# Performance work log

Hardware: AMD Instinct MI355X
Metric: run time of the kernel (lower is better)

The kernel has to match this reference:

```python
import jax, jax.numpy as jnp
import numpy as np

# DeepSeek MLA prefill pipeline (absorbed form), matching the GEMM/bmm/sparse-attention
# Dims: m=512 tokens, hidden=7168, d_kv_c=512, d_q_c=1536, d_r=64, d_q=d_kv=128,
# h=16 local heads, attention dim d = d_kv_c + d_r = 576, s_kv=4096, topk=512.

M, HID = 512, 7168
D_KV_C, D_Q_C, D_R, D_Q, D_KV = 512, 1536, 64, 128, 128
H = 16
S_KV, TOPK = 4096, 512
D_ATT = D_KV_C + D_R  # 576


def setup_inputs() -> dict:
    key = jax.random.key(0)
    ks = jax.random.split(key, 8)
    s = lambda n: 1.0 / np.sqrt(n).astype(np.float32)
    return {
        "x": jax.random.normal(ks[0], (M, HID), jnp.float32),
        "W_cqkv": jax.random.normal(ks[1], (HID, D_KV_C + D_Q_C + D_R), jnp.float32) * s(HID),
        "W_uq": jax.random.normal(ks[2], (D_Q_C, H * (D_Q + D_R)), jnp.float32) * s(D_Q_C),
        "W_qk": jax.random.normal(ks[3], (H, D_Q, D_KV_C), jnp.float32) * s(D_Q),
        "kv_cache": jax.random.normal(ks[4], (S_KV, D_ATT), jnp.float32),
        "W_o1": jax.random.normal(ks[5], (H, D_KV_C, D_KV), jnp.float32) * s(D_KV_C),
        "W_oproj": jax.random.normal(ks[6], (H * D_KV, HID), jnp.float32) * s(H * D_KV),
        "indices": jax.random.randint(ks[7], (M, TOPK), 0, S_KV, jnp.int32),
    }


def reference(x, W_cqkv, W_uq, W_qk, kv_cache, W_o1, W_oproj, indices):
    # 1) QKV compression GEMM: [m, hid] @ [hid, d_kv_c + d_q_c + d_r]
    c = x @ W_cqkv
    kv_c_new = c[:, :D_KV_C]                      # compressed KV (would extend cache)
    q_c = c[:, D_KV_C:D_KV_C + D_Q_C]             # [m, d_q_c]
    # (kv_c_new / k_r_new feed the cache in a real pipeline; attention below reads

    # 2) Q uncompression GEMM: [m, d_q_c] @ [d_q_c, h*(d_q+d_r)]
    q = (q_c @ W_uq).reshape(M, H, D_Q + D_R)
    q_nope, q_pe = q[..., :D_Q], q[..., D_Q:]     # [m,h,128], [m,h,64]

    # 3) Q absorb bmm: per-head [m, d_q] @ [d_q, d_kv_c]
    q_abs = jnp.einsum('mhq,hqc->mhc', q_nope, W_qk)
    q_full = jnp.concatenate([q_abs, q_pe], axis=-1)  # [m, h, 576]

    # 4) Top-k sparse MLA attention (flash_mla_sparse_fwd math):
    #    indices shared across heads (h_kv = 1); gather kv rows per query token.
    kv_g = kv_cache[indices]                      # [m, topk, 576]
    sm_scale = 1.0 / jnp.sqrt(jnp.float32(D_ATT))
    scores = jnp.einsum('mhd,mtd->mht', q_full, kv_g) * sm_scale
    attn = jax.nn.softmax(scores, axis=-1)        # [m, h, topk]
    o = jnp.einsum('mht,mtc->mhc', attn, kv_g[..., :D_KV_C])  # value = first d_kv_c dims

    # 5) O bmm: per-head [m, d_kv_c] @ [d_kv_c, d_kv]
    o2 = jnp.einsum('mhc,hcv->mhv', o, W_o1)      # [m, h, 128]

    # 6) O projection GEMM: [m, h*d_kv] @ [h*d_kv, hid]
    out = o2.reshape(M, H * D_KV) @ W_oproj       # [m, hid]
    return out
```

## Files before the change

### kernel.cpp

```cpp
#include <hip/hip_runtime.h>
#include <hip/hip_bf16.h>

#define M_DIM 512
#define HID 7168
#define D_KV_C 512
#define D_Q_C 1536
#define D_R 64
#define D_Q 128
#define D_KV 128
#define H_DIM 16
#define S_KV 4096
#define TOPK 512
#define D_ATT 576
#define SPLIT 2
#define SROWS 256
#define SM_SCALE (1.0f / 24.0f)

typedef _Float16 half_t;
typedef __attribute__((ext_vector_type(8))) _Float16 f16x8_t;
typedef __attribute__((ext_vector_type(4))) float f32x4_t;
typedef __attribute__((ext_vector_type(2))) unsigned int u32x2_t;

#define MFMA_F16(a, b, c) __builtin_amdgcn_mfma_f32_16x16x32_f16((a), (b), (c), 0, 0, 0)

__device__ __forceinline__ unsigned lds_addr32(const void* p) {
    return (unsigned)(unsigned long long)(const __attribute__((address_space(3))) char*)p;
}

typedef const __attribute__((address_space(1))) unsigned int* gptr_t;
typedef __attribute__((address_space(3))) unsigned int* lptr_t;
__device__ __forceinline__ void gload_lds16(const void* g, void* l) {
    __builtin_amdgcn_global_load_lds((gptr_t)g, (lptr_t)l, 16, 0, 0);
}

__global__ __launch_bounds__(256) void cvt_f16(const float* __restrict__ src,
                                               half_t* __restrict__ dst, int n8)
{
    int i = blockIdx.x * 256 + threadIdx.x;
    if (i >= n8) return;
    const float4* s = (const float4*)src + (size_t)i * 2;
    float4 a = s[0], b = s[1];
    f16x8_t o;
    o[0] = (half_t)a.x; o[1] = (half_t)a.y; o[2] = (half_t)a.z; o[3] = (half_t)a.w;
    o[4] = (half_t)b.x; o[5] = (half_t)b.y; o[6] = (half_t)b.z; o[7] = (half_t)b.w;
    *(f16x8_t*)(dst + (size_t)i * 8) = o;
}

template<int NS>
__global__ __launch_bounds__(256) void cvt_sum(const float* __restrict__ src, long long slice,
                                               half_t* __restrict__ dst, int n8)
{
    int i = blockIdx.x * 256 + threadIdx.x;
    if (i >= n8) return;
    float a[8] = {};
    #pragma unroll
    for (int s = 0; s < NS; s++) {
        const float4* p = (const float4*)(src + (size_t)s * slice) + (size_t)i * 2;
        float4 u = p[0], v = p[1];
        a[0] += u.x; a[1] += u.y; a[2] += u.z; a[3] += u.w;
        a[4] += v.x; a[5] += v.y; a[6] += v.z; a[7] += v.w;
    }
    f16x8_t o;
    #pragma unroll
    for (int j = 0; j < 8; j++) o[j] = (half_t)a[j];
    *(f16x8_t*)(dst + (size_t)i * 8) = o;
}

template<int NS>
__global__ __launch_bounds__(256) void cvt_sum_q(const float* __restrict__ src, long long slice,
                                                 half_t* __restrict__ q16, half_t* __restrict__ qf)
{
    int i = blockIdx.x * 256 + threadIdx.x;
    if (i >= M_DIM * 3072 / 8) return;
    float a[8] = {};
    #pragma unroll
    for (int s = 0; s < NS; s++) {
        const float4* p = (const float4*)(src + (size_t)s * slice) + (size_t)i * 2;
        float4 u = p[0], v = p[1];
        a[0] += u.x; a[1] += u.y; a[2] += u.z; a[3] += u.w;
        a[4] += v.x; a[5] += v.y; a[6] += v.z; a[7] += v.w;
    }
    f16x8_t o;
    #pragma unroll
    for (int j = 0; j < 8; j++) o[j] = (half_t)a[j];
    *(f16x8_t*)(q16 + (size_t)i * 8) = o;
    int col = (i * 8) % 3072;
    int c = col % 192;
    if (c >= 128) {
        int row = (i * 8) / 3072, h = col / 192;
        int mh = row * 16 + h;
        f16x8_t os;
        #pragma unroll
        for (int j = 0; j < 8; j++) os[j] = (half_t)(a[j] * SM_SCALE);
        *(f16x8_t*)(qf + (size_t)mh * D_ATT + D_KV_C + (c - 128)) = os;
    }
}

__global__ __launch_bounds__(256) void cvt_t(
    const float* __restrict__ src, int ld_src, long long sS,
    half_t* __restrict__ dst, int ld_dst, long long sD)
{
    src += (size_t)blockIdx.z * sS;
    dst += (size_t)blockIdx.z * sD;
    int k0 = blockIdx.y * 64, n0 = blockIdx.x * 64;
    __shared__ half_t t[64][80];
    int tid = threadIdx.x;
    int kr = tid >> 4, nc = (tid & 15) * 4;
    #pragma unroll
    for (int i = 0; i < 4; i++) {
        float4 v = *(const float4*)&src[(size_t)(k0 + kr + i * 16) * ld_src + n0 + nc];
        t[nc + 0][kr + i * 16] = (half_t)v.x;
        t[nc + 1][kr + i * 16] = (half_t)v.y;
        t[nc + 2][kr + i * 16] = (half_t)v.z;
        t[nc + 3][kr + i * 16] = (half_t)v.w;
    }
    __syncthreads();
    int nr = tid >> 2, kc = (tid & 3) * 16;
    f16x8_t w0 = *(const f16x8_t*)&t[nr][kc];
    f16x8_t w1 = *(const f16x8_t*)&t[nr][kc + 8];
    *(f16x8_t*)&dst[(size_t)(n0 + nr) * ld_dst + k0 + kc] = w0;
    *(f16x8_t*)&dst[(size_t)(n0 + nr) * ld_dst + k0 + kc + 8] = w1;
}

template<bool F16OUT>
__global__ __launch_bounds__(256) void gemm_f16t(
    const half_t* __restrict__ A, int lda, long long sA,
    const half_t* __restrict__ Bt, int ldb, long long sB,
    void* __restrict__ Cv, int ldc, long long sC, int K, float alpha)
{
    A  += (size_t)blockIdx.z * sA;
    Bt += (size_t)blockIdx.z * sB;
    const int bm = blockIdx.y * 64, bn = blockIdx.x * 64;

    __shared__ __align__(16) char lds[2][16384];

    const int tid = threadIdx.x, w = tid >> 6, lane = tid & 63;
    const int l15 = lane & 15, q = lane >> 4;
    const int wr = w >> 1, wc = w & 1;

    const half_t* gA[2];
    const half_t* gB[2];
    #pragma unroll
    for (int p = 0; p < 2; p++) {
        int c = p * 64 + lane;
        int rl = c >> 3;
        int sg = (c & 7) ^ (rl & 7);
        gA[p] = A  + (size_t)(bm + w * 16 + rl) * lda + sg * 8;
        gB[p] = Bt + (size_t)(bn + w * 16 + rl) * ldb + sg * 8;
    }

    f32x4_t acc[2][2];
    #pragma unroll
    for (int i = 0; i < 2; i++)
        #pragma unroll
        for (int j = 0; j < 2; j++) acc[i][j] = (f32x4_t){0.f, 0.f, 0.f, 0.f};

    const int nsteps = K >> 6;

    {
        char* ab = lds[0];
        char* bb = ab + 8192;
        #pragma unroll
        for (int p = 0; p < 2; p++) {
            gload_lds16(gA[p], ab + w * 2048 + p * 1024);
            gload_lds16(gB[p], bb + w * 2048 + p * 1024);
        }
    }
    __syncthreads();

    int cur = 0;
    for (int s = 0; s < nsteps; s++) {
        if (s + 1 < nsteps) {
            int k0 = (s + 1) << 6;
            char* ab = lds[cur ^ 1];
            char* bb = ab + 8192;
            #pragma unroll
            for (int p = 0; p < 2; p++) {
                gload_lds16(gA[p] + k0, ab + w * 2048 + p * 1024);
                gload_lds16(gB[p] + k0, bb + w * 2048 + p * 1024);
            }
        }
        {
            const char* ab = lds[cur];
            const char* bb = ab + 8192;
            #pragma unroll
            for (int kk = 0; kk < 2; kk++) {
                f16x8_t av[2], bv[2];
                #pragma unroll
                for (int i = 0; i < 2; i++) {
                    int ra = wr * 32 + i * 16 + l15;
                    av[i] = *(const f16x8_t*)(ab + ra * 128 + (((kk * 4 + q) ^ (ra & 7)) * 16));
                    int rb = wc * 32 + i * 16 + l15;
                    bv[i] = *(const f16x8_t*)(bb + rb * 128 + (((kk * 4 + q) ^ (rb & 7)) * 16));
                }
                #pragma unroll
                for (int i = 0; i < 2; i++)
                    #pragma unroll
                    for (int j = 0; j < 2; j++)
                        acc[i][j] = MFMA_F16(av[i], bv[j], acc[i][j]);
            }
        }
        __syncthreads();
        cur ^= 1;
    }

    half_t* Ch = (half_t*)Cv + (F16OUT ? (size_t)blockIdx.z * sC : 0);
    float*  Cf = (float*)Cv  + (F16OUT ? 0 : (size_t)blockIdx.z * sC);
    #pragma unroll
    for (int i = 0; i < 2; i++)
        #pragma unroll
        for (int j = 0; j < 2; j++)
            #pragma unroll
            for (int r = 0; r < 4; r++) {
                size_t row = bm + wr * 32 + i * 16 + q * 4 + r;
                size_t col = bn + wc * 32 + j * 16 + l15;
                float v = acc[i][j][r] * alpha;
                if (F16OUT) Ch[row * ldc + col] = (half_t)v;
                else        Cf[row * ldc + col] = v;
            }
}

template<bool F16OUT>
__global__ __launch_bounds__(512, 4) void gemm_f16t_big(
    const half_t* __restrict__ A, int lda, long long sA,
    const half_t* __restrict__ Bt, int ldb, long long sB,
    void* __restrict__ Cv, int ldc, long long sC, int K, float alpha)
{
    A  += (size_t)blockIdx.z * sA;
    Bt += (size_t)blockIdx.z * sB;
    const int bm = blockIdx.y * 128, bn = blockIdx.x * 128;

    __shared__ __align__(16) char lds[2][32768];

    const int tid = threadIdx.x, w = tid >> 6, lane = tid & 63;
    const int l15 = lane & 15, q = lane >> 4;
    const int wr = w >> 2, wc = w & 3;

    const half_t* gA[2];
    const half_t* gB[2];
    #pragma unroll
    for (int p = 0; p < 2; p++) {
        int c = p * 64 + lane;
        int rl = c >> 3;
        int sg = (c & 7) ^ (rl & 7);
        gA[p] = A  + (size_t)(bm + w * 16 + rl) * lda + sg * 8;
        gB[p] = Bt + (size_t)(bn + w * 16 + rl) * ldb + sg * 8;
    }

    f32x4_t acc[4][2];
    #pragma unroll
    for (int i = 0; i < 4; i++)
        #pragma unroll
        for (int j = 0; j < 2; j++) acc[i][j] = (f32x4_t){0.f, 0.f, 0.f, 0.f};

    const int nsteps = K >> 6;

    {
        char* ab = lds[0];
        char* bb = ab + 16384;
        #pragma unroll
        for (int p = 0; p < 2; p++) {
            gload_lds16(gA[p], ab + w * 2048 + p * 1024);
            gload_lds16(gB[p], bb + w * 2048 + p * 1024);
        }
    }
    __syncthreads();

    int cur = 0;
    for (int s = 0; s < nsteps; s++) {
        if (s + 1 < nsteps) {
            int k0 = (s + 1) << 6;
            char* ab = lds[cur ^ 1];
            char* bb = ab + 16384;
            #pragma unroll
            for (int p = 0; p < 2; p++) {
                gload_lds16(gA[p] + k0, ab + w * 2048 + p * 1024);
                gload_lds16(gB[p] + k0, bb + w * 2048 + p * 1024);
            }
        }
        {
            const char* ab = lds[cur];
            const char* bb = ab + 16384;
            #pragma unroll
            for (int kk = 0; kk < 2; kk++) {
                f16x8_t av[4], bv[2];
                #pragma unroll
                for (int i = 0; i < 4; i++) {
                    int ra = wr * 64 + i * 16 + l15;
                    av[i] = *(const f16x8_t*)(ab + ra * 128 + (((kk * 4 + q) ^ (ra & 7)) * 16));
                }
                #pragma unroll
                for (int j = 0; j < 2; j++) {
                    int rb = wc * 32 + j * 16 + l15;
                    bv[j] = *(const f16x8_t*)(bb + rb * 128 + (((kk * 4 + q) ^ (rb & 7)) * 16));
                }
                #pragma unroll
                for (int i = 0; i < 4; i++)
                    #pragma unroll
                    for (int j = 0; j < 2; j++)
                        acc[i][j] = MFMA_F16(av[i], bv[j], acc[i][j]);
            }
        }
        __syncthreads();
        cur ^= 1;
    }

    half_t* Ch = (half_t*)Cv + (F16OUT ? (size_t)blockIdx.z * sC : 0);
    float*  Cf = (float*)Cv  + (F16OUT ? 0 : (size_t)blockIdx.z * sC);
    #pragma unroll
    for (int i = 0; i < 4; i++)
        #pragma unroll
        for (int j = 0; j < 2; j++)
            #pragma unroll
            for (int r = 0; r < 4; r++) {
                size_t row = bm + wr * 64 + i * 16 + q * 4 + r;
                size_t col = bn + wc * 32 + j * 16 + l15;
                float v = acc[i][j][r] * alpha;
                if (F16OUT) Ch[row * ldc + col] = (half_t)v;
                else        Cf[row * ldc + col] = v;
            }
}

__global__ __launch_bounds__(512, 4) void attn_split(
    const half_t* __restrict__ qf,
    const half_t* __restrict__ kvb,
    const int* __restrict__ indices,
    half_t* __restrict__ op,
    float2* __restrict__ ml)
{
    const int m = blockIdx.x, sp = blockIdx.y;
    const int tid = threadIdx.x;
    const int w = tid >> 6, lane = tid & 63;
    const int l15 = lane & 15, q = lane >> 4;

    __shared__ __align__(16) char vbuf[2][32768];
    __shared__ __align__(16) unsigned short p_s[16 * SROWS];
    __shared__ float red_m[16][8];
    __shared__ float red_s[16][8];

    const int* idxp = indices + (size_t)m * TOPK + sp * SROWS;

    {
        #pragma unroll
        for (int j = 0; j < 4; j++) {
            int R = 4 * w + j;
            int grow = idxp[R];
            unsigned swz = (((unsigned)(R & 7)) << 4) ^ (((unsigned)((R >> 3) & 3)) << 5);
            const char* src = (const char*)(kvb + (size_t)grow * D_ATT) + (((unsigned)(16 * lane)) ^ swz);
            gload_lds16(src, vbuf[0] + R * 1024);
        }
    }

    const int rows0 = idxp[(w * 2 + 0) * 16 + l15];
    const int rows1 = idxp[(w * 2 + 1) * 16 + l15];

    f32x4_t acc0 = (f32x4_t){0.f, 0.f, 0.f, 0.f};
    f32x4_t acc1 = (f32x4_t){0.f, 0.f, 0.f, 0.f};

    const half_t* qp  = qf  + ((size_t)m * 16 + l15) * D_ATT + q * 8;
    const half_t* kp0 = kvb + (size_t)rows0 * D_ATT + q * 8;
    const half_t* kp1 = kvb + (size_t)rows1 * D_ATT + q * 8;

    #pragma unroll
    for (int kk = 0; kk < 18; kk++) {
        f16x8_t ah = *(const f16x8_t*)(qp  + kk * 32);
        f16x8_t b0 = *(const f16x8_t*)(kp0 + kk * 32);
        f16x8_t b1 = *(const f16x8_t*)(kp1 + kk * 32);
        acc0 = MFMA_F16(ah, b0, acc0);
        acc1 = MFMA_F16(ah, b1, acc1);
    }

    float gm[4], e0[4], e1[4];
    #pragma unroll
    for (int r = 0; r < 4; r++) {
        float mx = fmaxf(acc0[r], acc1[r]);
        #pragma unroll
        for (int off = 8; off; off >>= 1) mx = fmaxf(mx, __shfl_xor(mx, off, 16));
        if (l15 == 0) red_m[q * 4 + r][w] = mx;
    }
    __syncthreads();
    #pragma unroll
    for (int r = 0; r < 4; r++) {
        int h = q * 4 + r;
        float mx = red_m[h][0];
        #pragma unroll
        for (int ww = 1; ww < 8; ww++) mx = fmaxf(mx, red_m[h][ww]);
        gm[r] = mx;
        e0[r] = __expf(acc0[r] - mx);
        e1[r] = __expf(acc1[r] - mx);
        float s = e0[r] + e1[r];
        #pragma unroll
        for (int off = 8; off; off >>= 1) s += __shfl_xor(s, off, 16);
        if (l15 == 0) red_s[h][w] = s;
    }
    __syncthreads();
    if (w == 0 && l15 == 0) {
        #pragma unroll
        for (int r = 0; r < 4; r++) {
            int h = q * 4 + r;
            float s = 0.f;
            #pragma unroll
            for (int ww = 0; ww < 8; ww++) s += red_s[h][ww];
            ml[(size_t)sp * (M_DIM * H_DIM) + m * 16 + h] = make_float2(gm[r], s);
        }
    }
    #pragma unroll
    for (int r = 0; r < 4; r++) {
        int h = q * 4 + r;
        int t0 = (w * 2 + 0) * 16 + l15;
        int t1 = t0 + 16;
        union { half_t hh; unsigned short u; } c0, c1;
        c0.hh = (half_t)e0[r]; c1.hh = (half_t)e1[r];
        p_s[h * SROWS + ((((unsigned)(t0 * 2)) ^ (((unsigned)(h & 7)) << 4)) >> 1)] = c0.u;
        p_s[h * SROWS + ((((unsigned)(t1 * 2)) ^ (((unsigned)(h & 7)) << 4)) >> 1)] = c1.u;
    }
    __syncthreads();

    f32x4_t oacc[4];
    #pragma unroll
    for (int i = 0; i < 4; i++) oacc[i] = (f32x4_t){0.f, 0.f, 0.f, 0.f};

    const int row1 = q * 8 + (l15 >> 2);
    const int row2 = row1 + 4;
    const unsigned sw1 = (((unsigned)(row1 & 7)) << 4) ^ (((unsigned)((row1 >> 3) & 3)) << 5);
    const unsigned sw2 = (((unsigned)(row2 & 7)) << 4) ^ (((unsigned)((row2 >> 3) & 3)) << 5);
    const unsigned cbyte = (unsigned)((l15 & 3) * 8);

    #pragma unroll 1
    for (int ct = 0; ct < 8; ct++) {
        if (ct < 7) {
            #pragma unroll
            for (int j = 0; j < 4; j++) {
                int R = 4 * w + j;
                int grow = idxp[(ct + 1) * 32 + R];
                unsigned swz = (((unsigned)(R & 7)) << 4) ^ (((unsigned)((R >> 3) & 3)) << 5);
                const char* src = (const char*)(kvb + (size_t)grow * D_ATT) + (((unsigned)(16 * lane)) ^ swz);
                gload_lds16(src, vbuf[(ct + 1) & 1] + R * 1024);
            }
        }

        const unsigned vb = lds_addr32(vbuf[ct & 1]);

        f16x8_t pa;
        {
            unsigned pbyte = ((unsigned)(ct * 64 + q * 16)) ^ (((unsigned)(l15 & 7)) << 4);
            pa = *(const f16x8_t*)((const char*)p_s + l15 * (SROWS * 2) + pbyte);
        }

        u32x2_t blo[4], bhi[4];
        #pragma unroll
        for (int i = 0; i < 4; i++) {
            unsigned c2 = ((unsigned)((w * 4 + i) * 32)) + cbyte;
            unsigned a1 = vb + (unsigned)row1 * 1024u + (c2 ^ sw1);
            unsigned a2 = vb + (unsigned)row2 * 1024u + (c2 ^ sw2);
            asm volatile("ds_read_b64_tr_b16 %0, %1 offset:0" : "=v"(blo[i]) : "v"(a1) : "memory");
            asm volatile("ds_read_b64_tr_b16 %0, %1 offset:0" : "=v"(bhi[i]) : "v"(a2) : "memory");
        }
        asm volatile("s_waitcnt lgkmcnt(0)" ::: "memory");
        __builtin_amdgcn_sched_barrier(0);

        __builtin_amdgcn_s_setprio(1);
        #pragma unroll
        for (int i = 0; i < 4; i++) {
            union { f16x8_t s; struct { u32x2_t lo, hi; } u; } f;
            f.u.lo = blo[i]; f.u.hi = bhi[i];
            oacc[i] = MFMA_F16(pa, f.s, oacc[i]);
        }
        __builtin_amdgcn_s_setprio(0);

        __syncthreads();
    }

    half_t* ob = op + ((size_t)sp * M_DIM + m) * (H_DIM * D_KV_C);
    #pragma unroll
    for (int i = 0; i < 4; i++) {
        int c = (w * 4 + i) * 16 + l15;
        #pragma unroll
        for (int r = 0; r < 4; r++)
            ob[(size_t)(q * 4 + r) * D_KV_C + c] = (half_t)oacc[i][r];
    }
}

__global__ __launch_bounds__(256) void attn_merge(
    const half_t* __restrict__ op,
    const float2* __restrict__ ml,
    half_t* __restrict__ o)
{
    int idx = blockIdx.x * 256 + threadIdx.x;
    if (idx >= M_DIM * H_DIM * D_KV_C / 8) return;
    int mh = idx >> 6;
    int c8 = (idx & 63) * 8;
    float2 a = ml[mh];
    float2 b = ml[M_DIM * H_DIM + mh];
    float Mx = fmaxf(a.x, b.x);
    float w0 = __expf(a.x - Mx), w1 = __expf(b.x - Mx);
    float inv = 1.0f / (w0 * a.y + w1 * b.y);
    w0 *= inv; w1 *= inv;
    f16x8_t v0 = *(const f16x8_t*)(op + (size_t)mh * D_KV_C + c8);
    f16x8_t v1 = *(const f16x8_t*)(op + ((size_t)(M_DIM * H_DIM) + mh) * D_KV_C + c8);
    f16x8_t o8;
    #pragma unroll
    for (int j = 0; j < 8; j++)
        o8[j] = (half_t)(w0 * (float)v0[j] + w1 * (float)v1[j]);
    *(f16x8_t*)(o + (size_t)mh * D_KV_C + c8) = o8;
}

extern "C" void kernel_launch(void* const* d_in, const int* in_sizes, int n_in,
                              void* d_out, int out_size, void* d_ws, size_t ws_size,
                              hipStream_t stream)
{
    const float* x        = (const float*)d_in[0];
    const float* W_cqkv   = (const float*)d_in[1];
    const float* W_uq     = (const float*)d_in[2];
    const float* W_qk     = (const float*)d_in[3];
    const float* kv_cache = (const float*)d_in[4];
    const float* W_o1     = (const float*)d_in[5];
    const float* W_oproj  = (const float*)d_in[6];
    const int*   indices  = (const int*)d_in[7];
    float* out = (float*)d_out;

    half_t* wsh = (half_t*)d_ws;
    half_t* Wcqkv_t = wsh;
    half_t* qc16    = wsh;
    half_t* o_part  = wsh;
    half_t* q32h    = wsh + 786432;
    half_t* q16     = wsh + 13369344;
    half_t* x16     = wsh + 11010048;
    half_t* o2_16   = wsh + 11010048;
    half_t* Wuq_t   = wsh + 14680064;
    half_t* o16     = wsh + 14680064;
    half_t* Wqk_t   = wsh + 19398656;
    half_t* ml_h    = wsh + 19398656;
    half_t* Wo1_t   = wsh + 20447232;
    half_t* Wop_t   = wsh + 21495808;
    half_t* kv16    = wsh + 36175872;
    half_t* qc32h   = wsh + 38535168;
    half_t* qf16    = wsh + 38535168;
    float*  qc32 = (float*)qc32h;
    float*  q32  = (float*)q32h;
    float2* ml   = (float2*)ml_h;

    cvt_f16<<<(M_DIM * HID / 8 + 255) / 256, 256, 0, stream>>>(x, x16, M_DIM * HID / 8);
    cvt_f16<<<(S_KV * D_ATT / 8 + 255) / 256, 256, 0, stream>>>(kv_cache, kv16, S_KV * D_ATT / 8);
    cvt_t<<<dim3(D_Q_C / 64, HID / 64, 1), 256, 0, stream>>>(
        W_cqkv + D_KV_C, D_KV_C + D_Q_C + D_R, 0, Wcqkv_t, HID, 0);
    cvt_t<<<dim3(3072 / 64, D_Q_C / 64, 1), 256, 0, stream>>>(
        W_uq, 3072, 0, Wuq_t, D_Q_C, 0);
    cvt_t<<<dim3(D_KV_C / 64, D_Q / 64, H_DIM), 256, 0, stream>>>(
        W_qk, D_KV_C, D_Q * D_KV_C, Wqk_t, D_Q, D_Q * D_KV_C);
    cvt_t<<<dim3(D_KV / 64, D_KV_C / 64, H_DIM), 256, 0, stream>>>(
        W_o1, D_KV, D_KV_C * D_KV, Wo1_t, D_KV_C, D_KV_C * D_KV);
    cvt_t<<<dim3(HID / 64, 2048 / 64, 1), 256, 0, stream>>>(
        W_oproj, HID, 0, Wop_t, 2048, 0);

    gemm_f16t_big<false><<<dim3(D_Q_C / 128, M_DIM / 128, 4), 512, 0, stream>>>(
        x16, HID, 1792, Wcqkv_t, HID, 1792, qc32, D_Q_C, (long long)M_DIM * D_Q_C, 1792, 1.0f);
    cvt_sum<4><<<(M_DIM * D_Q_C / 8 + 255) / 256, 256, 0, stream>>>(
        qc32, (long long)M_DIM * D_Q_C, qc16, M_DIM * D_Q_C / 8);

    gemm_f16t_big<false><<<dim3(3072 / 128, M_DIM / 128, 4), 512, 0, stream>>>(
        qc16, D_Q_C, 384, Wuq_t, D_Q_C, 384, q32, 3072, (long long)M_DIM * 3072, 384, 1.0f);
    cvt_sum_q<4><<<(M_DIM * 3072 / 8 + 255) / 256, 256, 0, stream>>>(
        q32, (long long)M_DIM * 3072, q16, qf16);

    gemm_f16t<true><<<dim3(D_KV_C / 64, M_DIM / 64, H_DIM), 256, 0, stream>>>(
        q16, 3072, D_Q + D_R, Wqk_t, D_Q, (long long)D_Q * D_KV_C,
        qf16, H_DIM * D_ATT, D_ATT, D_Q, SM_SCALE);

    attn_split<<<dim3(M_DIM, SPLIT), 512, 0, stream>>>(qf16, kv16, indices, o_part, ml);
    attn_merge<<<(M_DIM * H_DIM * D_KV_C / 8 + 255) / 256, 256, 0, stream>>>(o_part, ml, o16);

    gemm_f16t<true><<<dim3(D_KV / 64, M_DIM / 64, H_DIM), 256, 0, stream>>>(
        o16, H_DIM * D_KV_C, D_KV_C, Wo1_t, D_KV_C, (long long)D_KV_C * D_KV,
        o2_16, H_DIM * D_KV, D_KV, D_KV_C, 1.0f);

    gemm_f16t_big<false><<<dim3(HID / 128, M_DIM / 128, 1), 512, 0, stream>>>(
        o2_16, H_DIM * D_KV, 0, Wop_t, 2048, 0, out, HID, 0, 2048, 1.0f);
}
```

Before: 222.6 us.

## Stage full gathered KV rows in LDS once and split attention four ways

The sparse attention kernel now splits the top-k rows into four chunks of 128 instead of two of 256. Each block gathers all 576 columns of its 128 KV rows into LDS at once and reuses that copy for both the QK score MFMAs and the PV transposed reads. This removes the duplicate global reads of K for scores and the per-tile double-buffer syncs. The cost is more LDS per block (launch bounds lowered to 2 blocks), more blocks, and a merge kernel that combines four partials in place, which required moving workspace buffers.

After: 239.8 us. +7.7%, slower.

```diff
diff --git a/kernel.cpp b/kernel.cpp
--- a/kernel.cpp
+++ b/kernel.cpp
@@ -12,8 +12,8 @@
 #define S_KV 4096
 #define TOPK 512
 #define D_ATT 576
-#define SPLIT 2
-#define SROWS 256
+#define SPLIT 4
+#define SROWS 128
 #define SM_SCALE (1.0f / 24.0f)
 
 typedef _Float16 half_t;
@@ -321,7 +321,7 @@
             }
 }
 
-__global__ __launch_bounds__(512, 4) void attn_split(
+__global__ __launch_bounds__(512, 2) void attn_split(
     const half_t* __restrict__ qf,
     const half_t* __restrict__ kvb,
     const int* __restrict__ indices,
@@ -333,47 +333,43 @@
     const int w = tid >> 6, lane = tid & 63;
     const int l15 = lane & 15, q = lane >> 4;
 
-    __shared__ __align__(16) char vbuf[2][32768];
+    __shared__ __align__(16) char kbuf[SROWS * 1152];
     __shared__ __align__(16) unsigned short p_s[16 * SROWS];
     __shared__ float red_m[16][8];
     __shared__ float red_s[16][8];
 
     const int* idxp = indices + (size_t)m * TOPK + sp * SROWS;
 
-    {
-        #pragma unroll
-        for (int j = 0; j < 4; j++) {
-            int R = 4 * w + j;
-            int grow = idxp[R];
-            unsigned swz = (((unsigned)(R & 7)) << 4) ^ (((unsigned)((R >> 3) & 3)) << 5);
-            const char* src = (const char*)(kvb + (size_t)grow * D_ATT) + (((unsigned)(16 * lane)) ^ swz);
-            gload_lds16(src, vbuf[0] + R * 1024);
-        }
-    }
-
-    const int rows0 = idxp[(w * 2 + 0) * 16 + l15];
-    const int rows1 = idxp[(w * 2 + 1) * 16 + l15];
+    #pragma unroll
+    for (int i = 0; i < 18; i++) {
+        int cbase = i * 512 + w * 64;
+        int c = cbase + lane;
+        int R = c / 72;
+        int xo = (c - R * 72) * 16;
+        unsigned swz = (((unsigned)(R & 7)) << 4) ^ (((unsigned)((R >> 3) & 3)) << 5);
+        const char* src = (const char*)(kvb + (size_t)idxp[R] * D_ATT) + (((unsigned)xo) ^ swz);
+        gload_lds16(src, kbuf + (size_t)cbase * 16);
+    }
+
+    const int R0 = w * 16 + l15;
+    const unsigned swzR = (((unsigned)(R0 & 7)) << 4) ^ (((unsigned)((R0 >> 3) & 3)) << 5);
+    const half_t* qp = qf + ((size_t)m * 16 + l15) * D_ATT + q * 8;
 
     f32x4_t acc0 = (f32x4_t){0.f, 0.f, 0.f, 0.f};
-    f32x4_t acc1 = (f32x4_t){0.f, 0.f, 0.f, 0.f};
-
-    const half_t* qp  = qf  + ((size_t)m * 16 + l15) * D_ATT + q * 8;
-    const half_t* kp0 = kvb + (size_t)rows0 * D_ATT + q * 8;
-    const half_t* kp1 = kvb + (size_t)rows1 * D_ATT + q * 8;
+
+    __syncthreads();
 
     #pragma unroll
     for (int kk = 0; kk < 18; kk++) {
-        f16x8_t ah = *(const f16x8_t*)(qp  + kk * 32);
-        f16x8_t b0 = *(const f16x8_t*)(kp0 + kk * 32);
-        f16x8_t b1 = *(const f16x8_t*)(kp1 + kk * 32);
+        f16x8_t ah = *(const f16x8_t*)(qp + kk * 32);
+        f16x8_t b0 = *(const f16x8_t*)(kbuf + R0 * 1152 + (((unsigned)(kk * 64 + q * 16)) ^ swzR));
         acc0 = MFMA_F16(ah, b0, acc0);
-        acc1 = MFMA_F16(ah, b1, acc1);
-    }
-
-    float gm[4], e0[4], e1[4];
+    }
+
+    float gm[4], e0[4];
     #pragma unroll
     for (int r = 0; r < 4; r++) {
-        float mx = fmaxf(acc0[r], acc1[r]);
+        float mx = acc0[r];
         #pragma unroll
         for (int off = 8; off; off >>= 1) mx = fmaxf(mx, __shfl_xor(mx, off, 16));
         if (l15 == 0) red_m[q * 4 + r][w] = mx;
@@ -387,8 +383,7 @@
         for (int ww = 1; ww < 8; ww++) mx = fmaxf(mx, red_m[h][ww]);
         gm[r] = mx;
         e0[r] = __expf(acc0[r] - mx);
-        e1[r] = __expf(acc1[r] - mx);
-        float s = e0[r] + e1[r];
+        float s = e0[r];
         #pragma unroll
         for (int off = 8; off; off >>= 1) s += __shfl_xor(s, off, 16);
         if (l15 == 0) red_s[h][w] = s;
@@ -407,12 +402,10 @@
     #pragma unroll
     for (int r = 0; r < 4; r++) {
         int h = q * 4 + r;
-        int t0 = (w * 2 + 0) * 16 + l15;
-        int t1 = t0 + 16;
-        union { half_t hh; unsigned short u; } c0, c1;
-        c0.hh = (half_t)e0[r]; c1.hh = (half_t)e1[r];
+        int t0 = w * 16 + l15;
+        union { half_t hh; unsigned short u; } c0;
+        c0.hh = (half_t)e0[r];
         p_s[h * SROWS + ((((unsigned)(t0 * 2)) ^ (((unsigned)(h & 7)) << 4)) >> 1)] = c0.u;
-        p_s[h * SROWS + ((((unsigned)(t1 * 2)) ^ (((unsigned)(h & 7)) << 4)) >> 1)] = c1.u;
     }
     __syncthreads();
 
@@ -420,39 +413,30 @@
     #pragma unroll
     for (int i = 0; i < 4; i++) oacc[i] = (f32x4_t){0.f, 0.f, 0.f, 0.f};
 
-    const int row1 = q * 8 + (l15 >> 2);
-    const int row2 = row1 + 4;
-    const unsigned sw1 = (((unsigned)(row1 & 7)) << 4) ^ (((unsigned)((row1 >> 3) & 3)) << 5);
-    const unsigned sw2 = (((unsigned)(row2 & 7)) << 4) ^ (((unsigned)((row2 >> 3) & 3)) << 5);
+    const unsigned kb = lds_addr32(kbuf);
+    const int r1 = q * 8 + (l15 >> 2);
+    const int r2 = r1 + 4;
     const unsigned cbyte = (unsigned)((l15 & 3) * 8);
 
-    #pragma unroll 1
-    for (int ct = 0; ct < 8; ct++) {
-        if (ct < 7) {
-            #pragma unroll
-            for (int j = 0; j < 4; j++) {
-                int R = 4 * w + j;
-                int grow = idxp[(ct + 1) * 32 + R];
-                unsigned swz = (((unsigned)(R & 7)) << 4) ^ (((unsigned)((R >> 3) & 3)) << 5);
-                const char* src = (const char*)(kvb + (size_t)grow * D_ATT) + (((unsigned)(16 * lane)) ^ swz);
-                gload_lds16(src, vbuf[(ct + 1) & 1] + R * 1024);
-            }
-        }
-
-        const unsigned vb = lds_addr32(vbuf[ct & 1]);
-
+    #pragma unroll
+    for (int ct = 0; ct < 4; ct++) {
         f16x8_t pa;
         {
             unsigned pbyte = ((unsigned)(ct * 64 + q * 16)) ^ (((unsigned)(l15 & 7)) << 4);
             pa = *(const f16x8_t*)((const char*)p_s + l15 * (SROWS * 2) + pbyte);
         }
 
+        int Rg1 = ct * 32 + r1;
+        int Rg2 = ct * 32 + r2;
+        unsigned s1 = (((unsigned)(Rg1 & 7)) << 4) ^ (((unsigned)((Rg1 >> 3) & 3)) << 5);
+        unsigned s2 = (((unsigned)(Rg2 & 7)) << 4) ^ (((unsigned)((Rg2 >> 3) & 3)) << 5);
+
         u32x2_t blo[4], bhi[4];
         #pragma unroll
         for (int i = 0; i < 4; i++) {
             unsigned c2 = ((unsigned)((w * 4 + i) * 32)) + cbyte;
-            unsigned a1 = vb + (unsigned)row1 * 1024u + (c2 ^ sw1);
-            unsigned a2 = vb + (unsigned)row2 * 1024u + (c2 ^ sw2);
+            unsigned a1 = kb + (unsigned)Rg1 * 1152u + (c2 ^ s1);
+            unsigned a2 = kb + (unsigned)Rg2 * 1152u + (c2 ^ s2);
             asm volatile("ds_read_b64_tr_b16 %0, %1 offset:0" : "=v"(blo[i]) : "v"(a1) : "memory");
             asm volatile("ds_read_b64_tr_b16 %0, %1 offset:0" : "=v"(bhi[i]) : "v"(a2) : "memory");
         }
@@ -467,8 +451,6 @@
             oacc[i] = MFMA_F16(pa, f.s, oacc[i]);
         }
         __builtin_amdgcn_s_setprio(0);
-
-        __syncthreads();
     }
 
     half_t* ob = op + ((size_t)sp * M_DIM + m) * (H_DIM * D_KV_C);
@@ -482,27 +464,35 @@
 }
 
 __global__ __launch_bounds__(256) void attn_merge(
-    const half_t* __restrict__ op,
-    const float2* __restrict__ ml,
-    half_t* __restrict__ o)
+    half_t* __restrict__ op,
+    const float2* __restrict__ ml)
 {
     int idx = blockIdx.x * 256 + threadIdx.x;
     if (idx >= M_DIM * H_DIM * D_KV_C / 8) return;
     int mh = idx >> 6;
     int c8 = (idx & 63) * 8;
-    float2 a = ml[mh];
-    float2 b = ml[M_DIM * H_DIM + mh];
-    float Mx = fmaxf(a.x, b.x);
-    float w0 = __expf(a.x - Mx), w1 = __expf(b.x - Mx);
-    float inv = 1.0f / (w0 * a.y + w1 * b.y);
-    w0 *= inv; w1 *= inv;
-    f16x8_t v0 = *(const f16x8_t*)(op + (size_t)mh * D_KV_C + c8);
-    f16x8_t v1 = *(const f16x8_t*)(op + ((size_t)(M_DIM * H_DIM) + mh) * D_KV_C + c8);
+    float2 a[SPLIT];
+    #pragma unroll
+    for (int s = 0; s < SPLIT; s++) a[s] = ml[s * (M_DIM * H_DIM) + mh];
+    float Mx = a[0].x;
+    #pragma unroll
+    for (int s = 1; s < SPLIT; s++) Mx = fmaxf(Mx, a[s].x);
+    float ws[SPLIT], denom = 0.f;
+    #pragma unroll
+    for (int s = 0; s < SPLIT; s++) { ws[s] = __expf(a[s].x - Mx); denom += ws[s] * a[s].y; }
+    float inv = 1.0f / denom;
+    float acc[8] = {};
+    #pragma unroll
+    for (int s = 0; s < SPLIT; s++) {
+        f16x8_t v = *(const f16x8_t*)(op + ((size_t)s * (M_DIM * H_DIM) + mh) * D_KV_C + c8);
+        float wn = ws[s] * inv;
+        #pragma unroll
+        for (int j = 0; j < 8; j++) acc[j] += wn * (float)v[j];
+    }
     f16x8_t o8;
     #pragma unroll
-    for (int j = 0; j < 8; j++)
-        o8[j] = (half_t)(w0 * (float)v0[j] + w1 * (float)v1[j]);
-    *(f16x8_t*)(o + (size_t)mh * D_KV_C + c8) = o8;
+    for (int j = 0; j < 8; j++) o8[j] = (half_t)acc[j];
+    *(f16x8_t*)(op + (size_t)mh * D_KV_C + c8) = o8;
 }
 
 extern "C" void kernel_launch(void* const* d_in, const int* in_sizes, int n_in,
@@ -523,12 +513,12 @@
     half_t* Wcqkv_t = wsh;
     half_t* qc16    = wsh;
     half_t* o_part  = wsh;
+    half_t* o16     = wsh;
     half_t* q32h    = wsh + 786432;
     half_t* q16     = wsh + 13369344;
     half_t* x16     = wsh + 11010048;
-    half_t* o2_16   = wsh + 11010048;
+    half_t* o2_16   = wsh + 16777216;
     half_t* Wuq_t   = wsh + 14680064;
-    half_t* o16     = wsh + 14680064;
     half_t* Wqk_t   = wsh + 19398656;
     half_t* ml_h    = wsh + 19398656;
     half_t* Wo1_t   = wsh + 20447232;
@@ -568,7 +558,7 @@
         qf16, H_DIM * D_ATT, D_ATT, D_Q, SM_SCALE);
 
     attn_split<<<dim3(M_DIM, SPLIT), 512, 0, stream>>>(qf16, kv16, indices, o_part, ml);
-    attn_merge<<<(M_DIM * H_DIM * D_KV_C / 8 + 255) / 256, 256, 0, stream>>>(o_part, ml, o16);
+    attn_merge<<<(M_DIM * H_DIM * D_KV_C / 8 + 255) / 256, 256, 0, stream>>>(o_part, ml);
 
     gemm_f16t<true><<<dim3(D_KV / 64, M_DIM / 64, H_DIM), 256, 0, stream>>>(
         o16, H_DIM * D_KV_C, D_KV_C, Wo1_t, D_KV_C, (long long)D_KV_C * D_KV,
```
